# Kernel tuning notes

Measured on AMD Instinct MI355X. Metric: run time of the kernel, lower is better.

The kernel has to match this reference:

```python
import jax, jax.numpy as jnp
import numpy as np
import math

H, Dh, S = 8, 64, 3          # heads, dim per head, samples factor
B, T, N, K = 2, 12, 512, 16  # batch, time, nodes, local-adj width
F = H * Dh                   # features = 512
SN = int(S * math.log2(N))   # Sampled_Nodes = 27
EPS = 1e-5


def setup_inputs() -> dict:
    key = jax.random.key(0)
    ks = jax.random.split(key, 22)
    sc = 1.0 / math.sqrt(F)
    W = lambda k: jax.random.normal(k, (F, F), jnp.float32) * sc
    bb = lambda k: jax.random.normal(k, (F,), jnp.float32) * 0.01
    return {
        "x": jax.random.normal(ks[0], (B, T, N, F), jnp.float32),
        "spa_eigvalue": jax.random.normal(ks[1], (F,), jnp.float32) * 0.1,
        "spa_eigvec": jax.random.normal(ks[2], (N, F), jnp.float32) * 0.1,
        "tem_eigvalue": jax.random.normal(ks[3], (F,), jnp.float32) * 0.1,
        "tem_eigvec": jax.random.normal(ks[4], (N, F), jnp.float32) * 0.1,
        "localadj": jax.random.randint(ks[5], (N, K), 0, N),
        "Wq": W(ks[6]), "bq": bb(ks[7]),
        "Wk": W(ks[8]), "bk": bb(ks[9]),
        "Wv": W(ks[10]), "bv": bb(ks[11]),
        "Wo": W(ks[12]), "bo": bb(ks[13]),
        "w_proj": jax.random.normal(ks[14], (K,), jnp.float32) / math.sqrt(K),
        "b_proj": jax.random.normal(ks[15], (), jnp.float32) * 0.01,
        "gamma": jnp.ones((F,), jnp.float32),
        "beta": jnp.zeros((F,), jnp.float32),
        "W1": W(ks[16]), "b1": bb(ks[17]),
        "W2": W(ks[18]), "b2": bb(ks[19]),
    }


def _lin(v, Wm, bv):  # torch nn.Linear: y = x @ W^T + b, W is [out, in]
    return jnp.einsum('...i,oi->...o', v, Wm) + bv


def _ln(v, g=None, b=None):  # LayerNorm over last dim, eps=1e-5
    mu = jnp.mean(v, -1, keepdims=True)
    var = jnp.var(v, -1, keepdims=True)
    y = (v - mu) * jax.lax.rsqrt(var + EPS)
    return y * g + b if g is not None else y


def reference(x, spa_eigvalue, spa_eigvec, tem_eigvalue, tem_eigvec, localadj,
              Wq, bq, Wk, bk, Wv, bv, Wo, bo, w_proj, b_proj,
              gamma, beta, W1, b1, W2, b2):
    # eigvec @ diag(eigval) == row-wise scaling
    x_ = x + (spa_eigvec * spa_eigvalue + tem_eigvec * tem_eigvalue)
    to_heads = lambda v: v.reshape(B, T, N, H, Dh).transpose(3, 0, 1, 2, 4)  # [H,B,T,N,Dh]
    Qh = to_heads(_lin(x_, Wq, bq))
    Kh = to_heads(_lin(x_, Wk, bk))
    Vh = to_heads(_lin(x_, Wv, bv))
    # local-adjacency K sampling: [H,B,T,N,K,Dh]
    Ks = Kh[:, :, :, localadj, :]
    qks = jnp.einsum('hbtnd,hbtnkd->hbtnk', Qh, Ks)
    # importance score per query node via learned projection over K neighbors
    M = jnp.einsum('hbtnk,k->hbtn', qks, w_proj) + b_proj
    _, m_top = jax.lax.top_k(M, SN)                              # [H,B,T,SN]
    Qr = jnp.take_along_axis(Qh, m_top[..., None], axis=3)       # [H,B,T,SN,Dh]
    scores = jnp.einsum('hbtsd,hbtnd->hbtsn', Qr, Kh) / math.sqrt(Dh)
    attn = jax.nn.softmax(scores, axis=-1)                       # [H,B,T,SN,N]
    cp = jnp.argmax(attn, axis=-2)                               # best sampled query per key node [H,B,T,N]
    val = jnp.einsum('hbtsn,hbtnd->hbtsd', attn, Vh)             # [H,B,T,SN,Dh]
    out = jnp.take_along_axis(val, cp[..., None], axis=3)        # [H,B,T,N,Dh]
    out = out.transpose(1, 2, 3, 0, 4).reshape(B, T, N, F)       # merge heads
    v = _ln(_lin(out, Wo, bo), gamma, beta)
    h = jax.nn.relu(_lin(v, W1, b1))
    h = _lin(h, W2, b2) + v
    return _ln(h)
```

## Files before the change

### kernel.cpp

```cpp
#include <hip/hip_runtime.h>
#include <math.h>

#define H_    8
#define DH    64
#define NN    512
#define KADJ  16
#define FF    512
#define BTOT  24
#define ROWS  12288
#define SN_   27
#define EPS_  1e-5f

typedef short short8 __attribute__((ext_vector_type(8)));
typedef float f32x4  __attribute__((ext_vector_type(4)));

__device__ __forceinline__ ushort f2bf(float x) {
    uint u = __float_as_uint(x);
    u += 0x7FFFu + ((u >> 16) & 1u);
    return (ushort)(u >> 16);
}
__device__ __forceinline__ float bf2f(ushort h) {
    return __uint_as_float(((uint)h) << 16);
}

__device__ __forceinline__ void gload_lds16(const ushort* g, ushort* l) {
    __builtin_amdgcn_global_load_lds(
        (const __attribute__((address_space(1))) unsigned int*)g,
        (__attribute__((address_space(3))) unsigned int*)l,
        16, 0, 0);
}

__global__ __launch_bounds__(256) void add_pos_bf16(
    const float* __restrict__ x,
    const float* __restrict__ spa_val, const float* __restrict__ spa_vec,
    const float* __restrict__ tem_val, const float* __restrict__ tem_vec,
    ushort* __restrict__ xh, ushort* __restrict__ xl)
{
    int i = blockIdx.x * 256 + threadIdx.x;
    int f4  = i & 127;
    int row = i >> 7;
    int n   = row & (NN - 1);

    float4 xv = reinterpret_cast<const float4*>(x)[i];
    float4 sv = reinterpret_cast<const float4*>(spa_vec)[n * 128 + f4];
    float4 tv = reinterpret_cast<const float4*>(tem_vec)[n * 128 + f4];
    float4 se = reinterpret_cast<const float4*>(spa_val)[f4];
    float4 te = reinterpret_cast<const float4*>(tem_val)[f4];
    float r0 = xv.x + sv.x * se.x + tv.x * te.x;
    float r1 = xv.y + sv.y * se.y + tv.y * te.y;
    float r2 = xv.z + sv.z * se.z + tv.z * te.z;
    float r3 = xv.w + sv.w * se.w + tv.w * te.w;
    ushort h0 = f2bf(r0), h1 = f2bf(r1), h2 = f2bf(r2), h3 = f2bf(r3);
    reinterpret_cast<ushort4*>(xh)[i] = make_ushort4(h0, h1, h2, h3);
    reinterpret_cast<ushort4*>(xl)[i] = make_ushort4(
        f2bf(r0 - bf2f(h0)), f2bf(r1 - bf2f(h1)),
        f2bf(r2 - bf2f(h2)), f2bf(r3 - bf2f(h3)));
}

__global__ __launch_bounds__(256) void wconv_kernel(
    const float* __restrict__ w0, const float* __restrict__ w1,
    const float* __restrict__ w2, const float* __restrict__ w3,
    const float* __restrict__ w4, const float* __restrict__ w5,
    ushort* __restrict__ whi, ushort* __restrict__ wlo)
{
    const int wi = blockIdx.y;
    const float* W = wi == 0 ? w0 : wi == 1 ? w1 : wi == 2 ? w2 :
                     wi == 3 ? w3 : wi == 4 ? w4 : w5;
    int i = blockIdx.x * 256 + threadIdx.x;
    float4 v = reinterpret_cast<const float4*>(W)[i];
    ushort h0 = f2bf(v.x), h1 = f2bf(v.y), h2 = f2bf(v.z), h3 = f2bf(v.w);
    reinterpret_cast<ushort4*>(whi + (size_t)wi * 262144)[i] =
        make_ushort4(h0, h1, h2, h3);
    if (wi < 2) {
        reinterpret_cast<ushort4*>(wlo + (size_t)wi * 262144)[i] =
            make_ushort4(f2bf(v.x - bf2f(h0)), f2bf(v.y - bf2f(h1)),
                         f2bf(v.z - bf2f(h2)), f2bf(v.w - bf2f(h3)));
    }
}

#define GBM 64
#define GBN 128

template <int SPLIT, int EPI, int OUT>
__global__ __launch_bounds__(256, 2) void gemm_mfma2(
    const ushort* __restrict__ Ah, const ushort* __restrict__ Al,
    const ushort* __restrict__ Wh, const ushort* __restrict__ Wl,
    const float* __restrict__ bias, const float* __restrict__ addsrc,
    float* __restrict__ Cf, ushort* __restrict__ Cb, ushort* __restrict__ Cl)
{
    __shared__ ushort sA [SPLIT ? GBM * 64 : GBM * 128];
    __shared__ ushort sB [SPLIT ? GBN * 64 : GBN * 128];
    __shared__ ushort sAl2[SPLIT ? GBM * 64 : 8];
    __shared__ ushort sBl2[SPLIT ? GBN * 64 : 8];

    const int nx  = gridDim.x >> 3;
    const int bid = blockIdx.x;
    const int lt  = (bid & 7) * nx + (bid >> 3);
    const int rowBase = (lt >> 2) * GBM;
    const int colBase = (lt & 3) * GBN;

    const int tid  = threadIdx.x;
    const int lane = tid & 63;
    const int wid  = tid >> 6;
    const int q    = lane >> 4;
    const int fr   = lane & 15;
    const int wm   = wid & 1;
    const int wn   = wid >> 1;

    const int ROWW = SPLIT ? 64 : 128;
    const int kadv = ROWW;

    const ushort* asrcH[SPLIT ? 2 : 4];
    const ushort* bsrcH[SPLIT ? 4 : 8];
    const ushort* asrcL[SPLIT ? 2 : 1];
    const ushort* bsrcL[SPLIT ? 4 : 1];

    if (!SPLIT) {
        #pragma unroll
        for (int c = 0; c < 4; ++c) {
            const int p   = wid * 4096 + c * 1024 + lane * 16;
            const int row = p >> 8;
            const int ss  = ((p >> 4) & 15) ^ (row & 7);
            asrcH[c] = Ah + (size_t)(rowBase + row) * FF + ss * 8;
        }
        #pragma unroll
        for (int c = 0; c < 8; ++c) {
            const int p   = wid * 8192 + c * 1024 + lane * 16;
            const int row = p >> 8;
            const int ss  = ((p >> 4) & 15) ^ (row & 7);
            bsrcH[c] = Wh + (size_t)(colBase + row) * FF + ss * 8;
        }
    } else {
        #pragma unroll
        for (int c = 0; c < 2; ++c) {
            const int p   = wid * 2048 + c * 1024 + lane * 16;
            const int row = p >> 7;
            const int ss  = ((p >> 4) & 7) ^ (row & 7);
            asrcH[c] = Ah + (size_t)(rowBase + row) * FF + ss * 8;
            asrcL[c] = Al + (size_t)(rowBase + row) * FF + ss * 8;
        }
        #pragma unroll
        for (int c = 0; c < 4; ++c) {
            const int p   = wid * 4096 + c * 1024 + lane * 16;
            const int row = p >> 7;
            const int ss  = ((p >> 4) & 7) ^ (row & 7);
            bsrcH[c] = Wh + (size_t)(colBase + row) * FF + ss * 8;
            bsrcL[c] = Wl + (size_t)(colBase + row) * FF + ss * 8;
        }
    }

    f32x4 acc[2][4];
    #pragma unroll
    for (int mi = 0; mi < 2; ++mi)
        #pragma unroll
        for (int ni = 0; ni < 4; ++ni) acc[mi][ni] = (f32x4){0.f, 0.f, 0.f, 0.f};

    const int NSTEP = SPLIT ? 8 : 4;
    const int swz = fr & 7;

    for (int step = 0; step < NSTEP; ++step) {
        if (!SPLIT) {
            #pragma unroll
            for (int c = 0; c < 4; ++c) {
                gload_lds16(asrcH[c], &sA[wid * 2048 + c * 512]);
                asrcH[c] += kadv;
            }
            #pragma unroll
            for (int c = 0; c < 8; ++c) {
                gload_lds16(bsrcH[c], &sB[wid * 4096 + c * 512]);
                bsrcH[c] += kadv;
            }
        } else {
            #pragma unroll
            for (int c = 0; c < 2; ++c) {
                gload_lds16(asrcH[c], &sA  [wid * 1024 + c * 512]);
                gload_lds16(asrcL[c], &sAl2[wid * 1024 + c * 512]);
                asrcH[c] += kadv; asrcL[c] += kadv;
            }
            #pragma unroll
            for (int c = 0; c < 4; ++c) {
                gload_lds16(bsrcH[c], &sB  [wid * 2048 + c * 512]);
                gload_lds16(bsrcL[c], &sBl2[wid * 2048 + c * 512]);
                bsrcH[c] += kadv; bsrcL[c] += kadv;
            }
        }
        __syncthreads();

        if (!SPLIT) {
            #pragma unroll
            for (int ksub = 0; ksub < 4; ++ksub) {
                const int kq = (ksub * 4 + q) ^ swz;
                short8 af[2], bf[4];
                #pragma unroll
                for (int mi = 0; mi < 2; ++mi)
                    af[mi] = *(const short8*)&sA[(wm * 32 + mi * 16 + fr) * 128 +
                                                 (kq << 3)];
                #pragma unroll
                for (int ni = 0; ni < 4; ++ni)
                    bf[ni] = *(const short8*)&sB[(wn * 64 + ni * 16 + fr) * 128 +
                                                 (kq << 3)];
                #pragma unroll
                for (int mi = 0; mi < 2; ++mi)
                    #pragma unroll
                    for (int ni = 0; ni < 4; ++ni)
                        acc[mi][ni] = __builtin_amdgcn_mfma_f32_16x16x32_bf16(
                            af[mi], bf[ni], acc[mi][ni], 0, 0, 0);
            }
        } else {
            #pragma unroll
            for (int ksub = 0; ksub < 2; ++ksub) {
                const int kq = (ksub * 4 + q) ^ swz;
                short8 ah[2], bh[4], t[4];
                #pragma unroll
                for (int mi = 0; mi < 2; ++mi)
                    ah[mi] = *(const short8*)&sA[(wm * 32 + mi * 16 + fr) * 64 +
                                                 (kq << 3)];
                #pragma unroll
                for (int ni = 0; ni < 4; ++ni)
                    bh[ni] = *(const short8*)&sB[(wn * 64 + ni * 16 + fr) * 64 +
                                                 (kq << 3)];
                #pragma unroll
                for (int mi = 0; mi < 2; ++mi)
                    #pragma unroll
                    for (int ni = 0; ni < 4; ++ni)
                        acc[mi][ni] = __builtin_amdgcn_mfma_f32_16x16x32_bf16(
                            ah[mi], bh[ni], acc[mi][ni], 0, 0, 0);
                #pragma unroll
                for (int ni = 0; ni < 4; ++ni)
                    t[ni] = *(const short8*)&sBl2[(wn * 64 + ni * 16 + fr) * 64 +
                                                  (kq << 3)];
                #pragma unroll
                for (int mi = 0; mi < 2; ++mi)
                    #pragma unroll
                    for (int ni = 0; ni < 4; ++ni)
                        acc[mi][ni] = __builtin_amdgcn_mfma_f32_16x16x32_bf16(
                            ah[mi], t[ni], acc[mi][ni], 0, 0, 0);
                #pragma unroll
                for (int mi = 0; mi < 2; ++mi)
                    t[mi] = *(const short8*)&sAl2[(wm * 32 + mi * 16 + fr) * 64 +
                                                  (kq << 3)];
                #pragma unroll
                for (int mi = 0; mi < 2; ++mi)
                    #pragma unroll
                    for (int ni = 0; ni < 4; ++ni)
                        acc[mi][ni] = __builtin_amdgcn_mfma_f32_16x16x32_bf16(
                            t[mi], bh[ni], acc[mi][ni], 0, 0, 0);
            }
        }
        __syncthreads();
    }

    #pragma unroll
    for (int mi = 0; mi < 2; ++mi)
        #pragma unroll
        for (int ni = 0; ni < 4; ++ni) {
            const int col = colBase + wn * 64 + ni * 16 + fr;
            const float bcol = bias[col];
            #pragma unroll
            for (int r = 0; r < 4; ++r) {
                const int row = rowBase + wm * 32 + mi * 16 + q * 4 + r;
                float v = acc[mi][ni][r] + bcol;
                if (EPI == 1) v = fmaxf(v, 0.0f);
                if (EPI == 2) v += addsrc[(size_t)row * FF + col];
                const size_t idx = (size_t)row * FF + col;
                if (OUT == 0) Cf[idx] = v;
                if (OUT == 1) Cb[idx] = f2bf(v);
                if (OUT == 2) {
                    ushort hh = f2bf(v);
                    Cb[idx] = hh;
                    Cl[idx] = f2bf(v - bf2f(hh));
                }
            }
        }
}

__global__ __launch_bounds__(256) void qks_M_kernel(
    const ushort* __restrict__ Qh, const ushort* __restrict__ Ql,
    const ushort* __restrict__ Kh, const ushort* __restrict__ Kl,
    const int* __restrict__ adj, const float* __restrict__ w_proj,
    const float* __restrict__ b_proj, float* __restrict__ Mout)
{
    const int unit = blockIdx.x * 16 + (threadIdx.x >> 4);
    const int l16  = threadIdx.x & 15;
    const int n    = unit & (NN - 1);
    const int hbt  = unit >> 9;
    const int h    = hbt / BTOT;
    const int bt   = hbt - h * BTOT;

    const uint headbase = (uint)(bt * NN) * FF + h * DH + l16 * 4;
    const ushort* khB = Kh + headbase;
    const ushort* klB = Kl + headbase;

    const int   aj = adj[n * KADJ + l16];
    f32x4 acc = (f32x4){0.f, 0.f, 0.f, 0.f};

    #pragma unroll
    for (int k = 0; k < KADJ; ++k) {
        const int  j   = __shfl(aj, k, 16);
        const float wk = w_proj[k];
        const uint off = (uint)j * FF;
        uint2 hu = *(const uint2*)(khB + off);
        uint2 lu = *(const uint2*)(klB + off);
        float k0 = __uint_as_float(hu.x << 16) + __uint_as_float(lu.x << 16);
        float k1 = __uint_as_float(hu.x & 0xFFFF0000u) +
                   __uint_as_float(lu.x & 0xFFFF0000u);
        float k2 = __uint_as_float(hu.y << 16) + __uint_as_float(lu.y << 16);
        float k3 = __uint_as_float(hu.y & 0xFFFF0000u) +
                   __uint_as_float(lu.y & 0xFFFF0000u);
        acc[0] += wk * k0; acc[1] += wk * k1;
        acc[2] += wk * k2; acc[3] += wk * k3;
    }

    const uint qidx = headbase + (uint)n * FF;
    uint2 qhu = *(const uint2*)(Qh + qidx);
    uint2 qlu = *(const uint2*)(Ql + qidx);
    float q0 = __uint_as_float(qhu.x << 16) + __uint_as_float(qlu.x << 16);
    float q1 = __uint_as_float(qhu.x & 0xFFFF0000u) +
               __uint_as_float(qlu.x & 0xFFFF0000u);
    float q2 = __uint_as_float(qhu.y << 16) + __uint_as_float(qlu.y << 16);
    float q3 = __uint_as_float(qhu.y & 0xFFFF0000u) +
               __uint_as_float(qlu.y & 0xFFFF0000u);
    float t = q0 * acc[0] + q1 * acc[1] + q2 * acc[2] + q3 * acc[3];
    #pragma unroll
    for (int o = 1; o <= 8; o <<= 1) t += __shfl_xor(t, o);
    if (l16 == 0) Mout[unit] = t + b_proj[0];
}

__global__ __launch_bounds__(512) void topk_kernel(
    const float* __restrict__ M, int* __restrict__ mtop)
{
    __shared__ float vals[NN];
    const int g = blockIdx.x;
    const int n = threadIdx.x;
    const float m = M[(size_t)g * NN + n];
    vals[n] = m;
    __syncthreads();

    int cnt = 0;
    #pragma unroll 16
    for (int j = 0; j < NN; ++j) {
        const float vj = vals[j];
        cnt += (vj > m || (vj == m && j < n)) ? 1 : 0;
    }
    if (cnt < SN_) mtop[g * SN_ + cnt] = n;
}

__global__ __launch_bounds__(1024) void fused_attn(
    const ushort* __restrict__ Qh, const ushort* __restrict__ Ql,
    const ushort* __restrict__ Kh, const ushort* __restrict__ Kl,
    const ushort* __restrict__ Vb, const int* __restrict__ mtop,
    ushort* __restrict__ attnout)
{
    __shared__ ushort P_lds[32 * 512];
    __shared__ ushort Vt_lds[64 * 512];
    __shared__ float red0[16][32];
    __shared__ float red1[16][32];
    __shared__ float val2[2][32][68];
    __shared__ int   cp_lds[NN];
    __shared__ int   mt[32];

    const int g = blockIdx.x;
    const int h = g / BTOT, bt = g % BTOT;
    const int tid = threadIdx.x;
    const int wave = tid >> 6, lane = tid & 63;
    const int q = lane >> 4, c = lane & 15;
    const size_t base_bt = (size_t)bt * NN * FF;
    const int hcol = h * DH;

    if (tid < 32) mt[tid] = mtop[g * SN_ + (tid < SN_ ? tid : 0)];
    __syncthreads();

    const int n0 = wave * 32;
    short8 bfh[2][2], bfl[2][2];
    #pragma unroll
    for (int nt = 0; nt < 2; ++nt) {
        const size_t kp = base_bt + (size_t)(n0 + nt * 16 + c) * FF + hcol + q * 8;
        #pragma unroll
        for (int ks = 0; ks < 2; ++ks) {
            bfh[nt][ks] = *(const short8*)&Kh[kp + ks * 32];
            bfl[nt][ks] = *(const short8*)&Kl[kp + ks * 32];
        }
    }

    ushort4 vreg[2][4];
    #pragma unroll
    for (int i = 0; i < 2; ++i) {
        const int u  = tid + i * 1024;
        const int d4 = u & 15, ng = u >> 4;
        #pragma unroll
        for (int ii = 0; ii < 4; ++ii)
            vreg[i][ii] = *(const ushort4*)&Vb[base_bt +
                (size_t)(ng * 4 + ii) * FF + hcol + d4 * 4];
    }

    short8 afh[2][2], afl[2][2];
    #pragma unroll
    for (int m = 0; m < 2; ++m) {
        const int grow = mt[m * 16 + c];
        const size_t qp = base_bt + (size_t)grow * FF + hcol + q * 8;
        #pragma unroll
        for (int ks = 0; ks < 2; ++ks) {
            afh[m][ks] = *(const short8*)&Qh[qp + ks * 32];
            afl[m][ks] = *(const short8*)&Ql[qp + ks * 32];
        }
    }

    f32x4 sc[2][2];
    #pragma unroll
    for (int m = 0; m < 2; ++m)
        #pragma unroll
        for (int nt = 0; nt < 2; ++nt) sc[m][nt] = (f32x4){0.f, 0.f, 0.f, 0.f};
    #pragma unroll
    for (int ks = 0; ks < 2; ++ks)
        #pragma unroll
        for (int m = 0; m < 2; ++m)
            #pragma unroll
            for (int nt = 0; nt < 2; ++nt) {
                sc[m][nt] = __builtin_amdgcn_mfma_f32_16x16x32_bf16(
                    afh[m][ks], bfh[nt][ks], sc[m][nt], 0, 0, 0);
                sc[m][nt] = __builtin_amdgcn_mfma_f32_16x16x32_bf16(
                    afh[m][ks], bfl[nt][ks], sc[m][nt], 0, 0, 0);
                sc[m][nt] = __builtin_amdgcn_mfma_f32_16x16x32_bf16(
                    afl[m][ks], bfh[nt][ks], sc[m][nt], 0, 0, 0);
            }
    #pragma unroll
    for (int m = 0; m < 2; ++m)
        #pragma unroll
        for (int nt = 0; nt < 2; ++nt)
            #pragma unroll
            for (int r = 0; r < 4; ++r) sc[m][nt][r] *= 0.125f;

    float rmax[2][4];
    #pragma unroll
    for (int m = 0; m < 2; ++m)
        #pragma unroll
        for (int r = 0; r < 4; ++r)
            rmax[m][r] = fmaxf(sc[m][0][r], sc[m][1][r]);
    #pragma unroll
    for (int off = 1; off <= 8; off <<= 1)
        #pragma unroll
        for (int m = 0; m < 2; ++m)
            #pragma unroll
            for (int r = 0; r < 4; ++r)
                rmax[m][r] = fmaxf(rmax[m][r], __shfl_xor(rmax[m][r], off));
    if (c == 0) {
        #pragma unroll
        for (int m = 0; m < 2; ++m)
            #pragma unroll
            for (int r = 0; r < 4; ++r)
                red0[wave][m * 16 + q * 4 + r] = rmax[m][r];
    }
    __syncthreads();
    float gmax[2][4];
    #pragma unroll
    for (int m = 0; m < 2; ++m)
        #pragma unroll
        for (int r = 0; r < 4; ++r) {
            const int row = m * 16 + q * 4 + r;
            float v = red0[0][row];
            #pragma unroll
            for (int w = 1; w < 16; ++w) v = fmaxf(v, red0[w][row]);
            gmax[m][r] = v;
        }

    float rsum[2][4] = {};
    #pragma unroll
    for (int m = 0; m < 2; ++m)
        #pragma unroll
        for (int nt = 0; nt < 2; ++nt)
            #pragma unroll
            for (int r = 0; r < 4; ++r) {
                float e = expf(sc[m][nt][r] - gmax[m][r]);
                sc[m][nt][r] = e;
                rsum[m][r] += e;
            }
    #pragma unroll
    for (int off = 1; off <= 8; off <<= 1)
        #pragma unroll
        for (int m = 0; m < 2; ++m)
            #pragma unroll
            for (int r = 0; r < 4; ++r)
                rsum[m][r] += __shfl_xor(rsum[m][r], off);
    if (c == 0) {
        #pragma unroll
        for (int m = 0; m < 2; ++m)
            #pragma unroll
            for (int r = 0; r < 4; ++r)
                red1[wave][m * 16 + q * 4 + r] = rsum[m][r];
    }
    __syncthreads();
    #pragma unroll
    for (int m = 0; m < 2; ++m)
        #pragma unroll
        for (int r = 0; r < 4; ++r) {
            const int row = m * 16 + q * 4 + r;
            float s = red1[0][row];
            #pragma unroll
            for (int w = 1; w < 16; ++w) s += red1[w][row];
            const float inv = 1.0f / s;
            #pragma unroll
            for (int nt = 0; nt < 2; ++nt) sc[m][nt][r] *= inv;
        }

    #pragma unroll
    for (int nt = 0; nt < 2; ++nt) {
        float bv = -INFINITY;
        int bi = 1 << 30;
        #pragma unroll
        for (int m = 0; m < 2; ++m)
            #pragma unroll
            for (int r = 0; r < 4; ++r) {
                const int row = m * 16 + q * 4 + r;
                if (row < SN_) {
                    float v = sc[m][nt][r];
                    if (v > bv) { bv = v; bi = row; }
                }
            }
        #pragma unroll
        for (int off = 16; off <= 32; off <<= 1) {
            float ov = __shfl_xor(bv, off);
            int   oi = __shfl_xor(bi, off);
            if (ov > bv || (ov == bv && oi < bi)) { bv = ov; bi = oi; }
        }
        if (q == 0) cp_lds[n0 + nt * 16 + c] = bi;
    }

    #pragma unroll
    for (int m = 0; m < 2; ++m)
        #pragma unroll
        for (int nt = 0; nt < 2; ++nt)
            #pragma unroll
            for (int r = 0; r < 4; ++r) {
                const int row = m * 16 + q * 4 + r;
                const int col = n0 + nt * 16 + c;
                P_lds[(row * 512 + col) ^ ((row & 7) << 3)] = f2bf(sc[m][nt][r]);
            }

    #pragma unroll
    for (int i = 0; i < 2; ++i) {
        const int u  = tid + i * 1024;
        const int d4 = u & 15, ng = u >> 4;
        const int n0v = ng * 4;
        #pragma unroll
        for (int j = 0; j < 4; ++j) {
            const int d = d4 * 4 + j;
            ushort4 t;
            t.x = ((const ushort*)&vreg[i][0])[j];
            t.y = ((const ushort*)&vreg[i][1])[j];
            t.z = ((const ushort*)&vreg[i][2])[j];
            t.w = ((const ushort*)&vreg[i][3])[j];
            *(ushort4*)&Vt_lds[(d * 512 + n0v) ^ ((d & 7) << 3)] = t;
        }
    }
    __syncthreads();

    const int kh = wave >> 3, rem = wave & 7;
    const int msel = rem >> 2, dt = rem & 3;
    const int dcol = dt * 16 + c;
    const int prow = msel * 16 + c;
    const int pswz = (prow & 7) << 3;
    const int vswz = (dcol & 7) << 3;
    f32x4 acc = (f32x4){0.f, 0.f, 0.f, 0.f};
    #pragma unroll
    for (int ks8 = 0; ks8 < 8; ++ks8) {
        const int kstep = kh * 8 + ks8;
        short8 a = *(const short8*)&P_lds[(prow * 512 + kstep * 32 + q * 8) ^ pswz];
        short8 b = *(const short8*)&Vt_lds[(dcol * 512 + kstep * 32 + q * 8) ^ vswz];
        acc = __builtin_amdgcn_mfma_f32_16x16x32_bf16(a, b, acc, 0, 0, 0);
    }
    #pragma unroll
    for (int r = 0; r < 4; ++r)
        val2[kh][msel * 16 + q * 4 + r][dt * 16 + c] = acc[r];
    __syncthreads();

    #pragma unroll
    for (int pass = 0; pass < 4; ++pass) {
        const int n  = pass * 128 + (tid >> 3);
        const int s  = cp_lds[n];
        const int d0 = (tid & 7) * 8;
        float vr[8];
        #pragma unroll
        for (int j = 0; j < 8; ++j)
            vr[j] = val2[0][s][d0 + j] + val2[1][s][d0 + j];
        uint4 u;
        u.x = (uint)f2bf(vr[0]) | ((uint)f2bf(vr[1]) << 16);
        u.y = (uint)f2bf(vr[2]) | ((uint)f2bf(vr[3]) << 16);
        u.z = (uint)f2bf(vr[4]) | ((uint)f2bf(vr[5]) << 16);
        u.w = (uint)f2bf(vr[6]) | ((uint)f2bf(vr[7]) << 16);
        *(uint4*)(attnout + base_bt + (size_t)n * FF + hcol + d0) = u;
    }
}

template <int AFFINE, int BFOUT>
__global__ __launch_bounds__(256) void ln_kernel(
    const float* __restrict__ X, const float* __restrict__ g,
    const float* __restrict__ b, float* __restrict__ Yf,
    ushort* __restrict__ Yb, int rows)
{
    const int row = blockIdx.x * 4 + (threadIdx.x >> 6);
    if (row >= rows) return;
    const int lane = threadIdx.x & 63;
    const float4* x4 = reinterpret_cast<const float4*>(X + (size_t)row * FF);
    float4 a = x4[lane];
    float4 c = x4[lane + 64];
    float s = a.x + a.y + a.z + a.w + c.x + c.y + c.z + c.w;
    float q = a.x * a.x + a.y * a.y + a.z * a.z + a.w * a.w +
              c.x * c.x + c.y * c.y + c.z * c.z + c.w * c.w;
    #pragma unroll
    for (int o = 32; o; o >>= 1) {
        s += __shfl_xor(s, o);
        q += __shfl_xor(q, o);
    }
    const float mu   = s * (1.0f / FF);
    const float var  = q * (1.0f / FF) - mu * mu;
    const float rstd = 1.0f / sqrtf(var + EPS_);

    float4 ya, yc;
    ya.x = (a.x - mu) * rstd; ya.y = (a.y - mu) * rstd;
    ya.z = (a.z - mu) * rstd; ya.w = (a.w - mu) * rstd;
    yc.x = (c.x - mu) * rstd; yc.y = (c.y - mu) * rstd;
    yc.z = (c.z - mu) * rstd; yc.w = (c.w - mu) * rstd;
    if (AFFINE) {
        float4 ga = reinterpret_cast<const float4*>(g)[lane];
        float4 gc = reinterpret_cast<const float4*>(g)[lane + 64];
        float4 ba = reinterpret_cast<const float4*>(b)[lane];
        float4 bc = reinterpret_cast<const float4*>(b)[lane + 64];
        ya.x = ya.x * ga.x + ba.x; ya.y = ya.y * ga.y + ba.y;
        ya.z = ya.z * ga.z + ba.z; ya.w = ya.w * ga.w + ba.w;
        yc.x = yc.x * gc.x + bc.x; yc.y = yc.y * gc.y + bc.y;
        yc.z = yc.z * gc.z + bc.z; yc.w = yc.w * gc.w + bc.w;
    }
    float4* y4 = reinterpret_cast<float4*>(Yf + (size_t)row * FF);
    y4[lane]      = ya;
    y4[lane + 64] = yc;
    if (BFOUT) {
        ushort4* yb = reinterpret_cast<ushort4*>(Yb + (size_t)row * FF);
        yb[lane] = make_ushort4(f2bf(ya.x), f2bf(ya.y), f2bf(ya.z), f2bf(ya.w));
        yb[lane + 64] = make_ushort4(f2bf(yc.x), f2bf(yc.y), f2bf(yc.z), f2bf(yc.w));
    }
}

extern "C" void kernel_launch(void* const* d_in, const int* in_sizes, int n_in,
                              void* d_out, int out_size, void* d_ws, size_t ws_size,
                              hipStream_t stream)
{
    const float* x       = (const float*)d_in[0];
    const float* spa_val = (const float*)d_in[1];
    const float* spa_vec = (const float*)d_in[2];
    const float* tem_val = (const float*)d_in[3];
    const float* tem_vec = (const float*)d_in[4];
    const int*   adj     = (const int*)  d_in[5];
    const float* Wq = (const float*)d_in[6];  const float* bq = (const float*)d_in[7];
    const float* Wk = (const float*)d_in[8];  const float* bk = (const float*)d_in[9];
    const float* Wv = (const float*)d_in[10]; const float* bv = (const float*)d_in[11];
    const float* Wo = (const float*)d_in[12]; const float* bo = (const float*)d_in[13];
    const float* w_proj = (const float*)d_in[14];
    const float* b_proj = (const float*)d_in[15];
    const float* gamma  = (const float*)d_in[16];
    const float* beta   = (const float*)d_in[17];
    const float* W1 = (const float*)d_in[18]; const float* b1 = (const float*)d_in[19];
    const float* W2 = (const float*)d_in[20]; const float* b2 = (const float*)d_in[21];

    float* out = (float*)d_out;

    const size_t R = (size_t)ROWS * FF;

    ushort* ws_u = (ushort*)d_ws;
    ushort* bufQh = ws_u;
    ushort* bufQl = ws_u + R;
    ushort* bufKh = ws_u + 2 * R;
    ushort* bufKl = ws_u + 3 * R;
    ushort* bufVb = ws_u + 4 * R;
    ushort* whi   = ws_u + 5 * R;
    ushort* wlo   = whi + 6 * 262144;
    float*  Mbuf  = (float*)(wlo + 2 * 262144);
    int*    mtop  = (int*)(Mbuf + (size_t)H_ * BTOT * NN);

    float* o_f32 = (float*)bufQh;
    float* v_f32 = (float*)bufKh;
    float* h2_f32 = (float*)bufQh;

    ushort* xh  = (ushort*)d_out;
    ushort* xl  = xh + R;
    ushort* attnout = xh;
    ushort* vbf = xl;
    ushort* h1b = xh;

    add_pos_bf16<<<(ROWS * FF / 4) / 256, 256, 0, stream>>>(
        x, spa_val, spa_vec, tem_val, tem_vec, xh, xl);

    wconv_kernel<<<dim3(256, 6), 256, 0, stream>>>(Wq, Wk, Wv, Wo, W1, W2, whi, wlo);

    const int NG = (ROWS / GBM) * (FF / GBN);
    gemm_mfma2<1, 0, 2><<<NG, 256, 0, stream>>>(xh, xl, whi, wlo, bq, nullptr,
                                                nullptr, bufQh, bufQl);
    gemm_mfma2<1, 0, 2><<<NG, 256, 0, stream>>>(xh, xl, whi + 262144, wlo + 262144,
                                                bk, nullptr, nullptr, bufKh, bufKl);
    gemm_mfma2<0, 0, 1><<<NG, 256, 0, stream>>>(xh, nullptr, whi + 2 * 262144, nullptr,
                                                bv, nullptr, nullptr, bufVb, nullptr);

    qks_M_kernel<<<(H_ * BTOT * NN) / 16, 256, 0, stream>>>(
        bufQh, bufQl, bufKh, bufKl, adj, w_proj, b_proj, Mbuf);
    topk_kernel<<<H_ * BTOT, 512, 0, stream>>>(Mbuf, mtop);

    fused_attn<<<H_ * BTOT, 1024, 0, stream>>>(
        bufQh, bufQl, bufKh, bufKl, bufVb, mtop, attnout);

    gemm_mfma2<0, 0, 0><<<NG, 256, 0, stream>>>(attnout, nullptr, whi + 3 * 262144,
                                                nullptr, bo, nullptr, o_f32, nullptr, nullptr);
    ln_kernel<1, 1><<<ROWS / 4, 256, 0, stream>>>(o_f32, gamma, beta, v_f32, vbf, ROWS);
    gemm_mfma2<0, 1, 1><<<NG, 256, 0, stream>>>(vbf, nullptr, whi + 4 * 262144, nullptr,
                                                b1, nullptr, nullptr, h1b, nullptr);
    gemm_mfma2<0, 2, 0><<<NG, 256, 0, stream>>>(h1b, nullptr, whi + 5 * 262144, nullptr,
                                                b2, v_f32, h2_f32, nullptr, nullptr);
    ln_kernel<0, 0><<<ROWS / 4, 256, 0, stream>>>(h2_f32, nullptr, nullptr, out, nullptr, ROWS);
}
```

Baseline: 210.9 us.

## Fuse Q and K split-precision projections into one GEMM sharing A tiles

Replaces the two separate split-bf16 GEMM launches for Q and K with one kernel that loads the hi/lo activation tile once and computes both Q and K accumulators against their weight tiles. This halves activation reads for these projections and removes one launch, at the cost of more LDS and accumulator registers, which may lower occupancy. It also adds s_setprio raises around the MFMA sections in the attention kernels to favour matrix issue. The generic GEMM template is simplified to the non-split path only.

Result: no change. 211.7 us (+0.4%).

```diff
diff --git a/kernel.cpp b/kernel.cpp
--- a/kernel.cpp
+++ b/kernel.cpp
@@ -81,17 +81,17 @@
 #define GBM 64
 #define GBN 128
 
-template <int SPLIT, int EPI, int OUT>
-__global__ __launch_bounds__(256, 2) void gemm_mfma2(
-    const ushort* __restrict__ Ah, const ushort* __restrict__ Al,
-    const ushort* __restrict__ Wh, const ushort* __restrict__ Wl,
-    const float* __restrict__ bias, const float* __restrict__ addsrc,
-    float* __restrict__ Cf, ushort* __restrict__ Cb, ushort* __restrict__ Cl)
-{
-    __shared__ ushort sA [SPLIT ? GBM * 64 : GBM * 128];
-    __shared__ ushort sB [SPLIT ? GBN * 64 : GBN * 128];
-    __shared__ ushort sAl2[SPLIT ? GBM * 64 : 8];
-    __shared__ ushort sBl2[SPLIT ? GBN * 64 : 8];
+__global__ __launch_bounds__(256, 2) void gemm_qk(
+    const ushort* __restrict__ Axh, long aLo,
+    const ushort* __restrict__ Wh0, long wLo, long wK,
+    const float* __restrict__ bq, const float* __restrict__ bk,
+    ushort* __restrict__ Qh, ushort* __restrict__ Ql,
+    ushort* __restrict__ Kh, ushort* __restrict__ Kl)
+{
+    __shared__ ushort sAh[GBM * 64];
+    __shared__ ushort sAl[GBM * 64];
+    __shared__ ushort sBh[2][GBN * 64];
+    __shared__ ushort sBl[2][GBN * 64];
 
     const int nx  = gridDim.x >> 3;
     const int bid = blockIdx.x;
@@ -107,118 +107,70 @@
     const int wm   = wid & 1;
     const int wn   = wid >> 1;
 
-    const int ROWW = SPLIT ? 64 : 128;
-    const int kadv = ROWW;
-
-    const ushort* asrcH[SPLIT ? 2 : 4];
-    const ushort* bsrcH[SPLIT ? 4 : 8];
-    const ushort* asrcL[SPLIT ? 2 : 1];
-    const ushort* bsrcL[SPLIT ? 4 : 1];
-
-    if (!SPLIT) {
+    const ushort* asrc[2];
+    const ushort* bsrc[4];
+    #pragma unroll
+    for (int c = 0; c < 2; ++c) {
+        const int p   = wid * 2048 + c * 1024 + lane * 16;
+        const int row = p >> 7;
+        const int ss  = ((p >> 4) & 7) ^ (row & 7);
+        asrc[c] = Axh + (size_t)(rowBase + row) * FF + ss * 8;
+    }
+    #pragma unroll
+    for (int c = 0; c < 4; ++c) {
+        const int p   = wid * 4096 + c * 1024 + lane * 16;
+        const int row = p >> 7;
+        const int ss  = ((p >> 4) & 7) ^ (row & 7);
+        bsrc[c] = Wh0 + (size_t)(colBase + row) * FF + ss * 8;
+    }
+
+    f32x4 accQ[2][4], accK[2][4];
+    #pragma unroll
+    for (int mi = 0; mi < 2; ++mi)
+        #pragma unroll
+        for (int ni = 0; ni < 4; ++ni) {
+            accQ[mi][ni] = (f32x4){0.f, 0.f, 0.f, 0.f};
+            accK[mi][ni] = (f32x4){0.f, 0.f, 0.f, 0.f};
+        }
+
+    const int swz = fr & 7;
+
+    for (int step = 0; step < 8; ++step) {
+        #pragma unroll
+        for (int c = 0; c < 2; ++c) {
+            gload_lds16(asrc[c],       &sAh[wid * 1024 + c * 512]);
+            gload_lds16(asrc[c] + aLo, &sAl[wid * 1024 + c * 512]);
+            asrc[c] += 64;
+        }
         #pragma unroll
         for (int c = 0; c < 4; ++c) {
-            const int p   = wid * 4096 + c * 1024 + lane * 16;
-            const int row = p >> 8;
-            const int ss  = ((p >> 4) & 15) ^ (row & 7);
-            asrcH[c] = Ah + (size_t)(rowBase + row) * FF + ss * 8;
-        }
-        #pragma unroll
-        for (int c = 0; c < 8; ++c) {
-            const int p   = wid * 8192 + c * 1024 + lane * 16;
-            const int row = p >> 8;
-            const int ss  = ((p >> 4) & 15) ^ (row & 7);
-            bsrcH[c] = Wh + (size_t)(colBase + row) * FF + ss * 8;
-        }
-    } else {
-        #pragma unroll
-        for (int c = 0; c < 2; ++c) {
-            const int p   = wid * 2048 + c * 1024 + lane * 16;
-            const int row = p >> 7;
-            const int ss  = ((p >> 4) & 7) ^ (row & 7);
-            asrcH[c] = Ah + (size_t)(rowBase + row) * FF + ss * 8;
-            asrcL[c] = Al + (size_t)(rowBase + row) * FF + ss * 8;
-        }
-        #pragma unroll
-        for (int c = 0; c < 4; ++c) {
-            const int p   = wid * 4096 + c * 1024 + lane * 16;
-            const int row = p >> 7;
-            const int ss  = ((p >> 4) & 7) ^ (row & 7);
-            bsrcH[c] = Wh + (size_t)(colBase + row) * FF + ss * 8;
-            bsrcL[c] = Wl + (size_t)(colBase + row) * FF + ss * 8;
-        }
-    }
-
-    f32x4 acc[2][4];
-    #pragma unroll
-    for (int mi = 0; mi < 2; ++mi)
-        #pragma unroll
-        for (int ni = 0; ni < 4; ++ni) acc[mi][ni] = (f32x4){0.f, 0.f, 0.f, 0.f};
-
-    const int NSTEP = SPLIT ? 8 : 4;
-    const int swz = fr & 7;
-
-    for (int step = 0; step < NSTEP; ++step) {
-        if (!SPLIT) {
-            #pragma unroll
-            for (int c = 0; c < 4; ++c) {
-                gload_lds16(asrcH[c], &sA[wid * 2048 + c * 512]);
-                asrcH[c] += kadv;
+            gload_lds16(bsrc[c],            &sBh[0][wid * 2048 + c * 512]);
+            gload_lds16(bsrc[c] + wLo,      &sBl[0][wid * 2048 + c * 512]);
+            gload_lds16(bsrc[c] + wK,       &sBh[1][wid * 2048 + c * 512]);
+            gload_lds16(bsrc[c] + wK + wLo, &sBl[1][wid * 2048 + c * 512]);
+            bsrc[c] += 64;
+        }
+        __syncthreads();
+
+        #pragma unroll
+        for (int ksub = 0; ksub < 2; ++ksub) {
+            const int kq = (ksub * 4 + q) ^ swz;
+            short8 ah[2], al[2];
+            #pragma unroll
+            for (int mi = 0; mi < 2; ++mi) {
+                ah[mi] = *(const short8*)&sAh[(wm * 32 + mi * 16 + fr) * 64 + (kq << 3)];
+                al[mi] = *(const short8*)&sAl[(wm * 32 + mi * 16 + fr) * 64 + (kq << 3)];
             }
-            #pragma unroll
-            for (int c = 0; c < 8; ++c) {
-                gload_lds16(bsrcH[c], &sB[wid * 4096 + c * 512]);
-                bsrcH[c] += kadv;
-            }
-        } else {
-            #pragma unroll
-            for (int c = 0; c < 2; ++c) {
-                gload_lds16(asrcH[c], &sA  [wid * 1024 + c * 512]);
-                gload_lds16(asrcL[c], &sAl2[wid * 1024 + c * 512]);
-                asrcH[c] += kadv; asrcL[c] += kadv;
-            }
-            #pragma unroll
-            for (int c = 0; c < 4; ++c) {
-                gload_lds16(bsrcH[c], &sB  [wid * 2048 + c * 512]);
-                gload_lds16(bsrcL[c], &sBl2[wid * 2048 + c * 512]);
-                bsrcH[c] += kadv; bsrcL[c] += kadv;
-            }
-        }
-        __syncthreads();
-
-        if (!SPLIT) {
-            #pragma unroll
-            for (int ksub = 0; ksub < 4; ++ksub) {
-                const int kq = (ksub * 4 + q) ^ swz;
-                short8 af[2], bf[4];
+            __builtin_amdgcn_s_setprio(1);
+            #pragma unroll
+            for (int qk = 0; qk < 2; ++qk) {
+                short8 bh[4], bl[4];
                 #pragma unroll
-                for (int mi = 0; mi < 2; ++mi)
-                    af[mi] = *(const short8*)&sA[(wm * 32 + mi * 16 + fr) * 128 +
-                                                 (kq << 3)];
-                #pragma unroll
-                for (int ni = 0; ni < 4; ++ni)
-                    bf[ni] = *(const short8*)&sB[(wn * 64 + ni * 16 + fr) * 128 +
-                                                 (kq << 3)];
-                #pragma unroll
-                for (int mi = 0; mi < 2; ++mi)
-                    #pragma unroll
-                    for (int ni = 0; ni < 4; ++ni)
-                        acc[mi][ni] = __builtin_amdgcn_mfma_f32_16x16x32_bf16(
-                            af[mi], bf[ni], acc[mi][ni], 0, 0, 0);
-            }
-        } else {
-            #pragma unroll
-            for (int ksub = 0; ksub < 2; ++ksub) {
-                const int kq = (ksub * 4 + q) ^ swz;
-                short8 ah[2], bh[4], t[4];
-                #pragma unroll
-                for (int mi = 0; mi < 2; ++mi)
-                    ah[mi] = *(const short8*)&sA[(wm * 32 + mi * 16 + fr) * 64 +
-                                                 (kq << 3)];
-                #pragma unroll
-                for (int ni = 0; ni < 4; ++ni)
-                    bh[ni] = *(const short8*)&sB[(wn * 64 + ni * 16 + fr) * 64 +
-                                                 (kq << 3)];
+                for (int ni = 0; ni < 4; ++ni) {
+                    bh[ni] = *(const short8*)&sBh[qk][(wn * 64 + ni * 16 + fr) * 64 + (kq << 3)];
+                    bl[ni] = *(const short8*)&sBl[qk][(wn * 64 + ni * 16 + fr) * 64 + (kq << 3)];
+                }
+                f32x4 (*acc)[4] = qk == 0 ? accQ : accK;
                 #pragma unroll
                 for (int mi = 0; mi < 2; ++mi)
                     #pragma unroll
@@ -226,26 +178,123 @@
                         acc[mi][ni] = __builtin_amdgcn_mfma_f32_16x16x32_bf16(
                             ah[mi], bh[ni], acc[mi][ni], 0, 0, 0);
                 #pragma unroll
-                for (int ni = 0; ni < 4; ++ni)
-                    t[ni] = *(const short8*)&sBl2[(wn * 64 + ni * 16 + fr) * 64 +
-                                                  (kq << 3)];
+                for (int mi = 0; mi < 2; ++mi)
+                    #pragma unroll
+                    for (int ni = 0; ni < 4; ++ni)
+                        acc[mi][ni] = __builtin_amdgcn_mfma_f32_16x16x32_bf16(
+                            ah[mi], bl[ni], acc[mi][ni], 0, 0, 0);
                 #pragma unroll
                 for (int mi = 0; mi < 2; ++mi)
                     #pragma unroll
                     for (int ni = 0; ni < 4; ++ni)
                         acc[mi][ni] = __builtin_amdgcn_mfma_f32_16x16x32_bf16(
-                            ah[mi], t[ni], acc[mi][ni], 0, 0, 0);
+                            al[mi], bh[ni], acc[mi][ni], 0, 0, 0);
+            }
+            __builtin_amdgcn_s_setprio(0);
+        }
+        __syncthreads();
+    }
+
+    #pragma unroll
+    for (int mi = 0; mi < 2; ++mi)
+        #pragma unroll
+        for (int ni = 0; ni < 4; ++ni) {
+            const int col = colBase + wn * 64 + ni * 16 + fr;
+            const float bqc = bq[col];
+            const float bkc = bk[col];
+            #pragma unroll
+            for (int r = 0; r < 4; ++r) {
+                const int row = rowBase + wm * 32 + mi * 16 + q * 4 + r;
+                const size_t idx = (size_t)row * FF + col;
+                float vq = accQ[mi][ni][r] + bqc;
+                ushort hq = f2bf(vq);
+                Qh[idx] = hq;
+                Ql[idx] = f2bf(vq - bf2f(hq));
+                float vk = accK[mi][ni][r] + bkc;
+                ushort hk = f2bf(vk);
+                Kh[idx] = hk;
+                Kl[idx] = f2bf(vk - bf2f(hk));
+            }
+        }
+}
+
+template <int EPI, int OUT>
+__global__ __launch_bounds__(256, 2) void gemm_mfma2(
+    const ushort* __restrict__ Ah, const ushort* __restrict__ Wh,
+    const float* __restrict__ bias, const float* __restrict__ addsrc,
+    float* __restrict__ Cf, ushort* __restrict__ Cb)
+{
+    __shared__ ushort sA[GBM * 128];
+    __shared__ ushort sB[GBN * 128];
+
+    const int nx  = gridDim.x >> 3;
+    const int bid = blockIdx.x;
+    const int lt  = (bid & 7) * nx + (bid >> 3);
+    const int rowBase = (lt >> 2) * GBM;
+    const int colBase = (lt & 3) * GBN;
+
+    const int tid  = threadIdx.x;
+    const int lane = tid & 63;
+    const int wid  = tid >> 6;
+    const int q    = lane >> 4;
+    const int fr   = lane & 15;
+    const int wm   = wid & 1;
+    const int wn   = wid >> 1;
+
+    const ushort* asrc[4];
+    const ushort* bsrc[8];
+    #pragma unroll
+    for (int c = 0; c < 4; ++c) {
+        const int p   = wid * 4096 + c * 1024 + lane * 16;
+        const int row = p >> 8;
+        const int ss  = ((p >> 4) & 15) ^ (row & 7);
+        asrc[c] = Ah + (size_t)(rowBase + row) * FF + ss * 8;
+    }
+    #pragma unroll
+    for (int c = 0; c < 8; ++c) {
+        const int p   = wid * 8192 + c * 1024 + lane * 16;
+        const int row = p >> 8;
+        const int ss  = ((p >> 4) & 15) ^ (row & 7);
+        bsrc[c] = Wh + (size_t)(colBase + row) * FF + ss * 8;
+    }
+
+    f32x4 acc[2][4];
+    #pragma unroll
+    for (int mi = 0; mi < 2; ++mi)
+        #pragma unroll
+        for (int ni = 0; ni < 4; ++ni) acc[mi][ni] = (f32x4){0.f, 0.f, 0.f, 0.f};
+
+    const int swz = fr & 7;
+
+    for (int step = 0; step < 4; ++step) {
+        #pragma unroll
+        for (int c = 0; c < 4; ++c) {
+            gload_lds16(asrc[c], &sA[wid * 2048 + c * 512]);
+            asrc[c] += 128;
+        }
+        #pragma unroll
+        for (int c = 0; c < 8; ++c) {
+            gload_lds16(bsrc[c], &sB[wid * 4096 + c * 512]);
+            bsrc[c] += 128;
+        }
+        __syncthreads();
+
+        #pragma unroll
+        for (int ksub = 0; ksub < 4; ++ksub) {
+            const int kq = (ksub * 4 + q) ^ swz;
+            short8 af[2], bf[4];
+            #pragma unroll
+            for (int mi = 0; mi < 2; ++mi)
+                af[mi] = *(const short8*)&sA[(wm * 32 + mi * 16 + fr) * 128 + (kq << 3)];
+            #pragma unroll
+            for (int ni = 0; ni < 4; ++ni)
+                bf[ni] = *(const short8*)&sB[(wn * 64 + ni * 16 + fr) * 128 + (kq << 3)];
+            #pragma unroll
+            for (int mi = 0; mi < 2; ++mi)
                 #pragma unroll
-                for (int mi = 0; mi < 2; ++mi)
-                    t[mi] = *(const short8*)&sAl2[(wm * 32 + mi * 16 + fr) * 64 +
-                                                  (kq << 3)];
-                #pragma unroll
-                for (int mi = 0; mi < 2; ++mi)
-                    #pragma unroll
-                    for (int ni = 0; ni < 4; ++ni)
-                        acc[mi][ni] = __builtin_amdgcn_mfma_f32_16x16x32_bf16(
-                            t[mi], bh[ni], acc[mi][ni], 0, 0, 0);
-            }
+                for (int ni = 0; ni < 4; ++ni)
+                    acc[mi][ni] = __builtin_amdgcn_mfma_f32_16x16x32_bf16(
+                        af[mi], bf[ni], acc[mi][ni], 0, 0, 0);
         }
         __syncthreads();
     }
@@ -265,11 +314,6 @@
                 const size_t idx = (size_t)row * FF + col;
                 if (OUT == 0) Cf[idx] = v;
                 if (OUT == 1) Cb[idx] = f2bf(v);
-                if (OUT == 2) {
-                    ushort hh = f2bf(v);
-                    Cb[idx] = hh;
-                    Cl[idx] = f2bf(v - bf2f(hh));
-                }
             }
         }
 }
@@ -410,6 +454,7 @@
     for (int m = 0; m < 2; ++m)
         #pragma unroll
         for (int nt = 0; nt < 2; ++nt) sc[m][nt] = (f32x4){0.f, 0.f, 0.f, 0.f};
+    __builtin_amdgcn_s_setprio(1);
     #pragma unroll
     for (int ks = 0; ks < 2; ++ks)
         #pragma unroll
@@ -423,6 +468,7 @@
                 sc[m][nt] = __builtin_amdgcn_mfma_f32_16x16x32_bf16(
                     afl[m][ks], bfh[nt][ks], sc[m][nt], 0, 0, 0);
             }
+    __builtin_amdgcn_s_setprio(0);
     #pragma unroll
     for (int m = 0; m < 2; ++m)
         #pragma unroll
@@ -561,6 +607,7 @@
     const int pswz = (prow & 7) << 3;
     const int vswz = (dcol & 7) << 3;
     f32x4 acc = (f32x4){0.f, 0.f, 0.f, 0.f};
+    __builtin_amdgcn_s_setprio(1);
     #pragma unroll
     for (int ks8 = 0; ks8 < 8; ++ks8) {
         const int kstep = kh * 8 + ks8;
@@ -568,6 +615,7 @@
         short8 b = *(const short8*)&Vt_lds[(dcol * 512 + kstep * 32 + q * 8) ^ vswz];
         acc = __builtin_amdgcn_mfma_f32_16x16x32_bf16(a, b, acc, 0, 0, 0);
     }
+    __builtin_amdgcn_s_setprio(0);
     #pragma unroll
     for (int r = 0; r < 4; ++r)
         val2[kh][msel * 16 + q * 4 + r][dt * 16 + c] = acc[r];
@@ -692,12 +740,11 @@
     wconv_kernel<<<dim3(256, 6), 256, 0, stream>>>(Wq, Wk, Wv, Wo, W1, W2, whi, wlo);
 
     const int NG = (ROWS / GBM) * (FF / GBN);
-    gemm_mfma2<1, 0, 2><<<NG, 256, 0, stream>>>(xh, xl, whi, wlo, bq, nullptr,
-                                                nullptr, bufQh, bufQl);
-    gemm_mfma2<1, 0, 2><<<NG, 256, 0, stream>>>(xh, xl, whi + 262144, wlo + 262144,
-                                                bk, nullptr, nullptr, bufKh, bufKl);
-    gemm_mfma2<0, 0, 1><<<NG, 256, 0, stream>>>(xh, nullptr, whi + 2 * 262144, nullptr,
-                                                bv, nullptr, nullptr, bufVb, nullptr);
+    gemm_qk<<<NG, 256, 0, stream>>>(xh, (long)R,
+                                    whi, (long)(6 * 262144), (long)262144,
+                                    bq, bk, bufQh, bufQl, bufKh, bufKl);
+    gemm_mfma2<0, 1><<<NG, 256, 0, stream>>>(xh, whi + 2 * 262144, bv, nullptr,
+                                             nullptr, bufVb);
 
     qks_M_kernel<<<(H_ * BTOT * NN) / 16, 256, 0, stream>>>(
         bufQh, bufQl, bufKh, bufKl, adj, w_proj, b_proj, Mbuf);
@@ -706,12 +753,12 @@
     fused_attn<<<H_ * BTOT, 1024, 0, stream>>>(
         bufQh, bufQl, bufKh, bufKl, bufVb, mtop, attnout);
 
-    gemm_mfma2<0, 0, 0><<<NG, 256, 0, stream>>>(attnout, nullptr, whi + 3 * 262144,
-                                                nullptr, bo, nullptr, o_f32, nullptr, nullptr);
+    gemm_mfma2<0, 0><<<NG, 256, 0, stream>>>(attnout, whi + 3 * 262144, bo, nullptr,
+                                             o_f32, nullptr);
     ln_kernel<1, 1><<<ROWS / 4, 256, 0, stream>>>(o_f32, gamma, beta, v_f32, vbf, ROWS);
-    gemm_mfma2<0, 1, 1><<<NG, 256, 0, stream>>>(vbf, nullptr, whi + 4 * 262144, nullptr,
-                                                b1, nullptr, nullptr, h1b, nullptr);
-    gemm_mfma2<0, 2, 0><<<NG, 256, 0, stream>>>(h1b, nullptr, whi + 5 * 262144, nullptr,
-                                                b2, v_f32, h2_f32, nullptr, nullptr);
+    gemm_mfma2<1, 1><<<NG, 256, 0, stream>>>(vbf, whi + 4 * 262144, b1, nullptr,
+                                             nullptr, h1b);
+    gemm_mfma2<2, 0><<<NG, 256, 0, stream>>>(h1b, whi + 5 * 262144, b2, v_f32,
+                                             h2_f32, nullptr);
     ln_kernel<0, 0><<<ROWS / 4, 256, 0, stream>>>(h2_f32, nullptr, nullptr, out, nullptr, ROWS);
 }
```
